# Kernel tuning notes

Measured on AMD Instinct MI355X. Metric: run time of the kernel, lower is better.

## Reference

```python
import jax, jax.numpy as jnp
import numpy as np

N_NODES = 100000
N_EDGES = 1600000
N_GRAPHS = 100
HEADS = 8
OUT_CH = 16
IN_FEAT = 128
EPS = 1e-5
NEG_SLOPE = 0.2


def setup_inputs() -> dict:
    key = jax.random.key(0)
    ks = jax.random.split(key, 8)
    x = jax.random.normal(ks[0], (N_NODES, IN_FEAT), dtype=jnp.float32)
    edge_index = jax.random.randint(ks[1], (2, N_EDGES), 0, N_NODES, dtype=jnp.int64)
    batch = jnp.sort(jax.random.randint(ks[2], (N_NODES,), 0, N_GRAPHS, dtype=jnp.int64))
    bn_gamma = jnp.ones((IN_FEAT,), jnp.float32)
    bn_beta = jnp.zeros((IN_FEAT,), jnp.float32)
    W = jax.random.normal(ks[3], (IN_FEAT, HEADS * OUT_CH), dtype=jnp.float32) * (1.0 / np.sqrt(IN_FEAT))
    att_src = jax.random.normal(ks[4], (HEADS, OUT_CH), dtype=jnp.float32) * 0.1
    att_dst = jax.random.normal(ks[5], (HEADS, OUT_CH), dtype=jnp.float32) * 0.1
    bias = jnp.zeros((OUT_CH,), jnp.float32)
    return {"x": x, "edge_index": edge_index, "batch": batch,
            "bn_gamma": bn_gamma, "bn_beta": bn_beta, "W": W,
            "att_src": att_src, "att_dst": att_dst, "bias": bias}


def reference(x, edge_index, batch, bn_gamma, bn_beta, W, att_src, att_dst, bias):
    N = x.shape[0]
    # BatchNorm1d (training mode: batch statistics, biased variance)
    mean = jnp.mean(x, axis=0)
    var = jnp.var(x, axis=0)
    xn = (x - mean) * jax.lax.rsqrt(var + EPS) * bn_gamma + bn_beta

    # GATConv (heads=HEADS, concat=False), with self-loops as in PyG default
    loop = jnp.arange(N, dtype=edge_index.dtype)
    src = jnp.concatenate([edge_index[0], loop])  # [Et]
    dst = jnp.concatenate([edge_index[1], loop])  # [Et]

    h = (xn @ W).reshape(N, HEADS, OUT_CH)  # [N,H,C]
    a_src = jnp.einsum('nhc,hc->nh', h, att_src)  # [N,H]
    a_dst = jnp.einsum('nhc,hc->nh', h, att_dst)  # [N,H]

    e = a_src[src] + a_dst[dst]  # [Et,H]
    e = jnp.where(e > 0, e, NEG_SLOPE * e)  # leaky_relu(0.2)
    # scatter-softmax over destination node (self-loops => every segment nonempty)
    m = jax.ops.segment_max(e, dst, num_segments=N)  # [N,H]
    e = jnp.exp(e - m[dst])
    s = jax.ops.segment_sum(e, dst, num_segments=N)  # [N,H]
    alpha = e / s[dst]  # [Et,H]

    msg = alpha[:, :, None] * h[src]  # [Et,H,C]
    out = jax.ops.segment_sum(msg, dst, num_segments=N)  # [N,H,C]
    out = out.mean(axis=1) + bias  # concat=False -> head mean, [N,C]

    out = jax.nn.elu(out)

    # global_mean_pool over graph ids
    sums = jax.ops.segment_sum(out, batch, num_segments=N_GRAPHS)  # [G,C]
    cnt = jax.ops.segment_sum(jnp.ones((N,), out.dtype), batch, num_segments=N_GRAPHS)
    return sums / jnp.maximum(cnt, 1.0)[:, None]
```

## Files before the change

### kernel.cpp

```cpp
#include <hip/hip_runtime.h>
#include <hip/hip_bf16.h>
#include <hip/hip_fp16.h>


#define N_NODES 100000
#define N_EDGE  1600000
#define N_ET    1700000
#define N_G     100
#define HEADS   8
#define OUTC    16
#define EPS     1e-5f
#define NEG     0.2f
#define NB_BUCKETS 391
#define BCAP    4864
#define BNB     128
#define ABB     640
#define EPB     2657
#define ESLOTS  3
#define GEMMB   1563

typedef unsigned int uint;
typedef unsigned short ushort;
typedef float f32x2 __attribute__((ext_vector_type(2)));
typedef float f32x4 __attribute__((ext_vector_type(4)));
typedef __bf16 bf16x8 __attribute__((ext_vector_type(8)));

__device__ __forceinline__ float bf2f_lo(uint u){ union{uint i; float f;} c; c.i = u << 16; return c.f; }
__device__ __forceinline__ float bf2f_hi(uint u){ union{uint i; float f;} c; c.i = u & 0xffff0000u; return c.f; }
__device__ __forceinline__ float bf2f(ushort u){ union{uint i; float f;} c; c.i = ((uint)u) << 16; return c.f; }
__device__ __forceinline__ float scrub(float v){ return (v == v) ? v : 0.f; }

__device__ __forceinline__ ushort f2bf(float f){
  union{float ff; uint u;} c; c.ff = f;
  uint u = c.u;
  if ((u & 0x7fffffffu) > 0x7f800000u) u = 0;
  return (ushort)((u + 0x7fffu + ((u >> 16) & 1u)) >> 16);
}
__device__ __forceinline__ ushort bfsan(ushort u){
  return ((ushort)(u & 0x7fffu) > (ushort)0x7f80u) ? (ushort)0 : u;
}

__device__ __forceinline__ float ldf(const void* p, int i, int f32){
  return f32 ? ((const float*)p)[i] : bf2f(((const ushort*)p)[i]);
}
__device__ __forceinline__ int ldid(const int* p, int flat, int is64){
  return is64 ? p[2 * flat] : p[flat];
}

__global__ __launch_bounds__(1024) void k_front(const void* __restrict__ xraw,
                                                float* __restrict__ stats,
                                                const int* __restrict__ ei,
                                                int* __restrict__ bcnt,
                                                uint* __restrict__ pairBuf){
  int t = threadIdx.x;
  if (blockIdx.x < BNB){
    __shared__ int cdet;
    __shared__ float red[4][1024];
    if (t == 0) cdet = 0;
    __syncthreads();
    if (t < 256){
      uint w = ((const uint*)xraw)[t]; uint el = (w >> 7) & 0xffu;
      if (el != 0 && (el < 110 || el > 140)) atomicAdd(&cdet, 1);
    }
    __syncthreads();
    int f32 = cdet > 64;
    int c = t & 63;
    int c0 = c * 2;
    int rg = t >> 6;
    float s0 = 0.f, s1 = 0.f, q0 = 0.f, q1 = 0.f;
    if (f32){
      const float2* x2 = (const float2*)xraw;
      for (int r = blockIdx.x * 16 + rg; r < N_NODES; r += BNB * 16){
        float2 v = x2[r * 64 + c];
        float f0 = scrub(v.x), f1 = scrub(v.y);
        s0 += f0; q0 += f0 * f0;
        s1 += f1; q1 += f1 * f1;
      }
    } else {
      const uint* x2 = (const uint*)xraw;
      for (int r = blockIdx.x * 16 + rg; r < N_NODES; r += BNB * 16){
        uint v = x2[r * 64 + c];
        float f0 = scrub(bf2f_lo(v)), f1 = scrub(bf2f_hi(v));
        s0 += f0; q0 += f0 * f0;
        s1 += f1; q1 += f1 * f1;
      }
    }
    red[0][t] = s0; red[1][t] = q0; red[2][t] = s1; red[3][t] = q1;
    __syncthreads();
    if (t < 64){
      s0 = 0.f; q0 = 0.f; s1 = 0.f; q1 = 0.f;
#pragma unroll
      for (int k = 0; k < 16; k++){
        s0 += red[0][t + 64 * k];
        q0 += red[1][t + 64 * k];
        s1 += red[2][t + 64 * k];
        q1 += red[3][t + 64 * k];
      }
      atomicAdd(&stats[c0],       s0);
      atomicAdd(&stats[c0+1],     s1);
      atomicAdd(&stats[128+c0],   q0);
      atomicAdd(&stats[128+c0+1], q1);
    }
  } else {
    __shared__ int hist[NB_BUCKETS];
    __shared__ int base[NB_BUCKETS];
    __shared__ int cdet2;
    int bid = blockIdx.x - BNB;
    if (t == 0) cdet2 = 0;
    for (int i = t; i < NB_BUCKETS; i += 1024) hist[i] = 0;
    __syncthreads();
    if (t < 128){ if (ei[2 * t + 1] != 0) atomicAdd(&cdet2, 1); }
    __syncthreads();
    int is64 = cdet2 < 32;
    int e0 = bid * EPB, e1 = min(e0 + EPB, N_ET);
    uint preg[ESLOTS];
    int  breg[ESLOTS];
#pragma unroll
    for (int j = 0; j < ESLOTS; j++){
      int e = e0 + t + j * 1024;
      uint pk = 0; int b = -1;
      if (e < e1){
        int s, d;
        if (e < N_EDGE){ s = ldid(ei, e, is64); d = ldid(ei, N_EDGE + e, is64); }
        else { s = d = e - N_EDGE; }
        uint dd = (uint)d; if (dd >= N_NODES) dd = 0;
        uint ss = (uint)s; if (ss >= N_NODES) ss = 0;
        b = (int)(dd >> 8);
        pk = (ss << 8) | (dd & 255u);
        atomicAdd(&hist[b], 1);
      }
      preg[j] = pk; breg[j] = b;
    }
    __syncthreads();
    for (int i = t; i < NB_BUCKETS; i += 1024){
      int c = hist[i];
      base[i] = c ? atomicAdd(&bcnt[i], c) : 0;
      hist[i] = 0;
    }
    __syncthreads();
#pragma unroll
    for (int j = 0; j < ESLOTS; j++){
      int b = breg[j];
      if (b >= 0){
        int pos = base[b] + atomicAdd(&hist[b], 1);
        if ((uint)pos < BCAP) pairBuf[(size_t)b * BCAP + pos] = preg[j];
      }
    }
  }
}

__global__ __launch_bounds__(128) void k_prep(const float* __restrict__ stats,
                                              const void* __restrict__ gamma,
                                              const void* __restrict__ beta,
                                              const void* __restrict__ W,
                                              const uint* __restrict__ x32,
                                              const int* __restrict__ b32,
                                              ushort* __restrict__ Wpb,
                                              float* __restrict__ bp,
                                              int* __restrict__ flags){
  __shared__ int cnt[2];
  __shared__ float scl8[8], shf8[8];
  int t = threadIdx.x, bid = blockIdx.x;
  if (t < 2) cnt[t] = 0;
  __syncthreads();
  { uint w = x32[t];       uint el = (w >> 7) & 0xffu;
    if (el != 0 && (el < 110 || el > 140)) atomicAdd(&cnt[0], 1); }
  { uint w = x32[t + 128]; uint el = (w >> 7) & 0xffu;
    if (el != 0 && (el < 110 || el > 140)) atomicAdd(&cnt[0], 1); }
  if (bid == 0){ if (b32[98001 + 2 * t] != 0) atomicAdd(&cnt[1], 1); }
  __syncthreads();
  int f32 = cnt[0] > 64;
  if (bid == 0 && t == 0){
    flags[0] = f32;
    flags[1] = 0;
    flags[2] = cnt[1] < 32;
    flags[3] = 0;
  }
  if (t < 8){
    int c = bid * 8 + t;
    float mean = scrub(stats[c] * (1.0f / N_NODES));
    float var  = stats[128 + c] * (1.0f / N_NODES) - mean * mean;
    if (!(var > 0.f)) var = 0.f;
    float sc = scrub(ldf(gamma, c, f32)) * rsqrtf(var + EPS);
    sc = scrub(sc);
    scl8[t] = sc;
    shf8[t] = scrub(scrub(ldf(beta, c, f32)) - mean * sc);
  }
  __syncthreads();
  float bacc = 0.f;
#pragma unroll
  for (int j = 0; j < 8; j++){
    int c = bid * 8 + j;
    float w = scrub(ldf(W, c * 128 + t, f32));
    Wpb[t * 128 + (c & 7) + (((c >> 3) ^ (t & 15)) << 3)] = f2bf(scl8[j] * w);
    bacc += shf8[j] * w;
  }
  atomicAdd(&bp[t], scrub(bacc));
}

__global__ __launch_bounds__(256) void k_gemmC(const void* __restrict__ xraw,
                                               const ushort* __restrict__ Wpb,
                                               const float* __restrict__ bp,
                                               const void* __restrict__ att_src,
                                               const void* __restrict__ att_dst,
                                               const int* __restrict__ flags,
                                               unsigned char* __restrict__ h8,
                                               __half* __restrict__ a_src16,
                                               __half* __restrict__ a_dst16,
                                               const uint* __restrict__ pairBuf,
                                               const int* __restrict__ bcnt,
                                               int* __restrict__ offsets,
                                               int* __restrict__ csr){
  __shared__ __align__(16) char smem[33792];
  __shared__ float sSL[128], sDL[128], bpL[128];
  int t = threadIdx.x;
  if (blockIdx.x < NB_BUCKETS){
    int* sscan = (int*)smem;
    int* degL  = (int*)(smem + 2048);
    int* offL  = (int*)(smem + 3072);
    int* curL  = (int*)(smem + 4096);
    int b = blockIdx.x;
    sscan[t]       = (t < NB_BUCKETS) ? min(bcnt[t], BCAP) : 0;
    sscan[t + 256] = (t + 256 < NB_BUCKETS) ? min(bcnt[t + 256], BCAP) : 0;
    degL[t] = 0;
    __syncthreads();
    for (int off = 1; off < 512; off <<= 1){
      int a0 = (t >= off) ? sscan[t - off] : 0;
      int a1 = (t + 256 >= off) ? sscan[t + 256 - off] : 0;
      __syncthreads();
      sscan[t] += a0; sscan[t + 256] += a1;
      __syncthreads();
    }
    int gbase = (b == 0) ? 0 : sscan[b - 1];
    if (b == NB_BUCKETS - 1 && t == 0) offsets[N_NODES] = sscan[NB_BUCKETS - 1];
    int cnt = min(bcnt[b], BCAP);
    const uint* run = pairBuf + (size_t)b * BCAP;
    for (int i = t; i < cnt; i += 256)
      atomicAdd(&degL[run[i] & 255u], 1);
    __syncthreads();
    int v = degL[t];
    offL[t] = v;
    __syncthreads();
    for (int off = 1; off < 256; off <<= 1){
      int add = (t >= off) ? offL[t - off] : 0;
      __syncthreads();
      offL[t] += add;
      __syncthreads();
    }
    int excl = offL[t] - v;
    int node = (b << 8) + t;
    if (node < N_NODES) offsets[node] = gbase + excl;
    offL[t] = excl;
    curL[t] = 0;
    __syncthreads();
    for (int i = t; i < cnt; i += 256){
      uint e = run[i];
      int dl = e & 255u;
      int pos = atomicAdd(&curL[dl], 1);
      csr[gbase + offL[dl] + pos] = (int)(e >> 8);
    }
  } else {
    int f32 = flags[0];
    int wv = t >> 6, l = t & 63;
    int row0 = (blockIdx.x - NB_BUCKETS) * 64;
    if (t < 128){
      sSL[t] = scrub(ldf(att_src, t, f32));
      sDL[t] = scrub(ldf(att_dst, t, f32));
      bpL[t] = bp[t];
    }
    {
      const uint4* wsrc = (const uint4*)Wpb;
      uint4* wdst = (uint4*)smem;
#pragma unroll
      for (int i = 0; i < 8; i++)
        wdst[i * 256 + t] = wsrc[i * 256 + t];
    }
    __syncthreads();
    ushort* BsT = (ushort*)smem;

    f32x4 acc[8];
#pragma unroll
    for (int ct = 0; ct < 8; ct++) acc[ct] = (f32x4){0.f, 0.f, 0.f, 0.f};
    int arow = row0 + wv * 16 + (l & 15);
    int cr = min(arow, N_NODES - 1);
    int kg = (l >> 4) * 8;
    union AB { uint4 q; bf16x8 v; ushort u[8]; };
#pragma unroll
    for (int kc = 0; kc < 4; kc++){
      AB a;
      if (f32){
        const float* xr = (const float*)xraw + (size_t)cr * 128 + kc * 32 + kg;
        float4 p0 = *(const float4*)xr;
        float4 p1 = *(const float4*)(xr + 4);
        a.u[0] = f2bf(p0.x); a.u[1] = f2bf(p0.y); a.u[2] = f2bf(p0.z); a.u[3] = f2bf(p0.w);
        a.u[4] = f2bf(p1.x); a.u[5] = f2bf(p1.y); a.u[6] = f2bf(p1.z); a.u[7] = f2bf(p1.w);
      } else {
        const ushort* xr = (const ushort*)xraw + (size_t)cr * 128 + kc * 32 + kg;
        a.q = *(const uint4*)xr;
#pragma unroll
        for (int j = 0; j < 8; j++) a.u[j] = bfsan(a.u[j]);
      }
#pragma unroll
      for (int ct = 0; ct < 8; ct++){
        int c = ct * 16 + (l & 15);
        int kb = kc * 4 + (l >> 4);
        AB bfr;
        bfr.q = *(const uint4*)(BsT + c * 128 + ((kb ^ (c & 15)) << 3));
        acc[ct] = __builtin_amdgcn_mfma_f32_16x16x32_bf16(a.v, bfr.v, acc[ct], 0, 0, 0);
      }
    }
    __syncthreads();
    float* Cs = (float*)smem;
#pragma unroll
    for (int ct = 0; ct < 8; ct++){
#pragma unroll
      for (int ri = 0; ri < 4; ri++)
        Cs[(wv * 16 + (l >> 4) * 4 + ri) * 132 + ct * 16 + (l & 15)] = acc[ct][ri];
    }
    __syncthreads();
    int row = t >> 2, cg = (t & 3) * 32;
    int r = row0 + row;
    if (r < N_NODES){
      float o[32];
#pragma unroll
      for (int i = 0; i < 8; i++){
        float4 v = *(const float4*)(Cs + row * 132 + cg + i * 4);
        o[i*4+0] = v.x; o[i*4+1] = v.y; o[i*4+2] = v.z; o[i*4+3] = v.w;
      }
#pragma unroll
      for (int j = 0; j < 32; j++){
        float v = scrub(o[j] + bpL[cg + j]);
        o[j] = fminf(fmaxf(v, -448.f), 448.f);
      }
      uint w[8];
#pragma unroll
      for (int i = 0; i < 8; i++){
        uint ww = __builtin_amdgcn_cvt_pk_fp8_f32(o[i*4+0], o[i*4+1], 0, false);
        w[i] = __builtin_amdgcn_cvt_pk_fp8_f32(o[i*4+2], o[i*4+3], (int)ww, true);
      }
      unsigned char* po = h8 + (size_t)r * 128 + cg;
      *(uint4*)po        = make_uint4(w[0], w[1], w[2], w[3]);
      *(uint4*)(po + 16) = make_uint4(w[4], w[5], w[6], w[7]);
      float s0 = 0.f, s1 = 0.f, d0 = 0.f, d1 = 0.f;
#pragma unroll
      for (int j = 0; j < 16; j++){
        s0 += o[j]      * sSL[cg + j];      d0 += o[j]      * sDL[cg + j];
        s1 += o[16 + j] * sSL[cg + 16 + j]; d1 += o[16 + j] * sDL[cg + 16 + j];
      }
      int hA = (t & 3) * 2;
      *(__half2*)(a_src16 + (size_t)r * 8 + hA) = __floats2half2_rn(scrub(s0), scrub(s1));
      *(__half2*)(a_dst16 + (size_t)r * 8 + hA) = __floats2half2_rn(scrub(d0), scrub(d1));
    }
  }
}

__global__ __launch_bounds__(256) void k_msg(const int* __restrict__ offsets, const int* __restrict__ csr,
                                             const __half* __restrict__ a_src16, const __half* __restrict__ a_dst16,
                                             const uint* __restrict__ h32, const void* __restrict__ bias,
                                             const int* __restrict__ flags,
                                             float* __restrict__ out_n){
  int f32 = flags[0];
  int t = threadIdx.x;
  int wv = t >> 6, lane = t & 63;
  int half = lane >> 5, li = lane & 31;
  int myh = li >> 2;
  int n = blockIdx.x * 4 + wv;
  int start = offsets[n], end = offsets[n + 1];
  float ad = __half2float(a_dst16[(size_t)n * 8 + myh]);
  const ushort* as16 = (const ushort*)a_src16;
  float acc0 = 0.f, acc1 = 0.f, acc2 = 0.f, acc3 = 0.f, den = 0.f;

#define PAIR(AA, HH)                                                  \
  { float e = __half2float(*(__half*)&(AA)) + ad;                     \
    e = fmaxf(e, NEG * e);                                            \
    float p = __expf(fminf(e, 30.f));                                 \
    f32x2 lo = __builtin_amdgcn_cvt_pk_f32_fp8((int)(HH), false);     \
    f32x2 hi = __builtin_amdgcn_cvt_pk_f32_fp8((int)(HH), true);      \
    den += p; acc0 += p * lo[0]; acc1 += p * lo[1];                   \
    acc2 += p * hi[0]; acc3 += p * hi[1]; }

  for (int base = start; base < end; base += 64){
    int cnt = min(64, end - base);
    int sreg = csr[min(base + lane, N_ET - 1)];
    int npair = cnt >> 1;
    int jj = 0;
    for (; jj + 4 <= npair; jj += 4){
      int i0 = 2 * jj + half;
      int s0 = __shfl(sreg, i0);
      int s1 = __shfl(sreg, i0 + 2);
      int s2 = __shfl(sreg, i0 + 4);
      int s3 = __shfl(sreg, i0 + 6);
      uint h0 = h32[(uint)s0 * 32u + li];
      uint h1 = h32[(uint)s1 * 32u + li];
      uint h2 = h32[(uint)s2 * 32u + li];
      uint h3 = h32[(uint)s3 * 32u + li];
      ushort a0 = as16[(uint)s0 * 8u + myh];
      ushort a1 = as16[(uint)s1 * 8u + myh];
      ushort a2 = as16[(uint)s2 * 8u + myh];
      ushort a3 = as16[(uint)s3 * 8u + myh];
      __builtin_amdgcn_sched_barrier(0);
      PAIR(a0, h0) PAIR(a1, h1) PAIR(a2, h2) PAIR(a3, h3)
    }
    for (; jj < npair; jj++){
      int s0 = __shfl(sreg, 2 * jj + half);
      uint h0 = h32[(uint)s0 * 32u + li];
      ushort a0 = as16[(uint)s0 * 8u + myh];
      PAIR(a0, h0)
    }
    if (cnt & 1){
      int sl = __shfl(sreg, cnt - 1);
      uint hh = h32[(uint)sl * 32u + li];
      ushort aa = as16[(uint)sl * 8u + myh];
      float e = __half2float(*(__half*)&aa) + ad;
      e = fmaxf(e, NEG * e);
      float p = __expf(fminf(e, 30.f));
      p = half ? 0.f : p;
      f32x2 lo = __builtin_amdgcn_cvt_pk_f32_fp8((int)hh, false);
      f32x2 hi = __builtin_amdgcn_cvt_pk_f32_fp8((int)hh, true);
      den += p; acc0 += p * lo[0]; acc1 += p * lo[1];
      acc2 += p * hi[0]; acc3 += p * hi[1];
    }
  }
#undef PAIR

  den  += __shfl_xor(den, 32);
  acc0 += __shfl_xor(acc0, 32);
  acc1 += __shfl_xor(acc1, 32);
  acc2 += __shfl_xor(acc2, 32);
  acc3 += __shfl_xor(acc3, 32);
  float inv = (den > 0.f) ? (1.0f / den) : 0.f;
  float v0 = acc0 * inv, v1 = acc1 * inv, v2 = acc2 * inv, v3 = acc3 * inv;
  v0 += __shfl_xor(v0, 4);  v1 += __shfl_xor(v1, 4);  v2 += __shfl_xor(v2, 4);  v3 += __shfl_xor(v3, 4);
  v0 += __shfl_xor(v0, 8);  v1 += __shfl_xor(v1, 8);  v2 += __shfl_xor(v2, 8);  v3 += __shfl_xor(v3, 8);
  v0 += __shfl_xor(v0, 16); v1 += __shfl_xor(v1, 16); v2 += __shfl_xor(v2, 16); v3 += __shfl_xor(v3, 16);
  if (lane < 4){
    int c0 = lane * 4;
    float o0 = v0 * 0.125f + scrub(ldf(bias, c0 + 0, f32));
    float o1 = v1 * 0.125f + scrub(ldf(bias, c0 + 1, f32));
    float o2 = v2 * 0.125f + scrub(ldf(bias, c0 + 2, f32));
    float o3 = v3 * 0.125f + scrub(ldf(bias, c0 + 3, f32));
    o0 = o0 > 0.f ? o0 : (__expf(o0) - 1.0f);
    o1 = o1 > 0.f ? o1 : (__expf(o1) - 1.0f);
    o2 = o2 > 0.f ? o2 : (__expf(o2) - 1.0f);
    o3 = o3 > 0.f ? o3 : (__expf(o3) - 1.0f);
    float4* po = (float4*)(out_n + (size_t)n * 16 + c0);
    *po = make_float4(scrub(o0), scrub(o1), scrub(o2), scrub(o3));
  }
}

__global__ __launch_bounds__(256) void k_pool(const float* __restrict__ out_n,
                                              const int* __restrict__ batch,
                                              const int* __restrict__ flags,
                                              float* __restrict__ out){
  int b64 = flags[2];
  int g = blockIdx.x;
  int t = threadIdx.x;
  int c = t & 15, rg = t >> 4;
  int lo = 0, hi = N_NODES;
  while (lo < hi){ int m = (lo + hi) >> 1; if (ldid(batch, m, b64) < g) lo = m + 1; else hi = m; }
  int lo2 = lo, hi2 = N_NODES;
  while (lo2 < hi2){ int m = (lo2 + hi2) >> 1; if (ldid(batch, m, b64) < g + 1) lo2 = m + 1; else hi2 = m; }
  float acc = 0.f;
  for (int r = lo + rg; r < lo2; r += 16)
    acc += out_n[(size_t)r * 16 + c];
  __shared__ float red[16][17];
  red[rg][c] = acc;
  __syncthreads();
  if (t < 16){
    float v = 0.f;
#pragma unroll
    for (int i = 0; i < 16; i++) v += red[i][t];
    float cntf = (float)(lo2 - lo);
    out[g * 16 + t] = scrub(v / fmaxf(cntf, 1.0f));
  }
}

extern "C" void kernel_launch(void* const* d_in, const int* in_sizes, int n_in,
                              void* d_out, int out_size, void* d_ws, size_t ws_size,
                              hipStream_t stream){
  (void)in_sizes; (void)n_in; (void)out_size; (void)ws_size;
  const void* x     = d_in[0];
  const int*  ei    = (const int*)d_in[1];
  const int*  batch = (const int*)d_in[2];
  const void* gamma = d_in[3];
  const void* beta  = d_in[4];
  const void* W     = d_in[5];
  const void* att_s = d_in[6];
  const void* att_d = d_in[7];
  const void* bias  = d_in[8];

  char* ws = (char*)d_ws;
  size_t off = 0;
  auto alloc = [&](size_t b){ size_t r = off; off += (b + 255) & ~(size_t)255; return r; };
  int*    flags   = (int*)(ws + alloc(4 * 4));
  float*  stats   = (float*)(ws + alloc(256 * 4));
  float*  bp      = (float*)(ws + alloc(128 * 4));
  int*    bcnt    = (int*)(ws + alloc(NB_BUCKETS * 4));
  size_t  zero_end = off;
  ushort* Wpb     = (ushort*)(ws + alloc(16384 * 2));
  int*    offsets = (int*)(ws + alloc((size_t)(N_NODES + 1) * 4));
  __half* a_src16 = (__half*)(ws + alloc((size_t)N_NODES * 8 * 2));
  __half* a_dst16 = (__half*)(ws + alloc((size_t)N_NODES * 8 * 2));
  size_t  pb_bytes = (size_t)NB_BUCKETS * BCAP * 4;
  size_t  on_bytes = (size_t)N_NODES * 16 * 4;
  char*   pb_region = ws + alloc(pb_bytes > on_bytes ? pb_bytes : on_bytes);
  uint*   pairBuf = (uint*)pb_region;
  float*  out_n   = (float*)pb_region;
  unsigned char* h8 = (unsigned char*)(ws + alloc((size_t)N_NODES * 128));
  int*    csr     = (int*)(ws + alloc((size_t)N_ET * 4));

  hipMemsetAsync(ws, 0, zero_end, stream);

  k_front<<<BNB + ABB, 1024, 0, stream>>>(x, stats, ei, bcnt, pairBuf);
  k_prep<<<16, 128, 0, stream>>>(stats, gamma, beta, W, (const uint*)x, batch, Wpb, bp, flags);
  k_gemmC<<<NB_BUCKETS + GEMMB, 256, 0, stream>>>(x, Wpb, bp, att_s, att_d, flags,
                                                  h8, a_src16, a_dst16,
                                                  pairBuf, bcnt, offsets, csr);
  k_msg<<<N_NODES / 4, 256, 0, stream>>>(offsets, csr, a_src16, a_dst16, (const uint*)h8, bias, flags, out_n);
  k_pool<<<N_G, 256, 0, stream>>>(out_n, batch, flags, (float*)d_out);
}
```

Before: 257.2 us.

## Split edge bucketing from BN stats and co-schedule it with half the GEMM

The edge-bucketing pass moves out of the BN statistics kernel into a new kernel that also runs the first half of the GEMM row tiles. The CSR build shares a launch with the remaining GEMM tiles. The bucketing blocks drop to 256 threads, each handling 12 edges with paired vectorized index loads. The aim is to overlap the memory-bound edge scatter with compute-bound GEMM work and to balance block mix across launches, at the cost of one extra launch and a split GEMM.

```diff
diff --git a/kernel.cpp b/kernel.cpp
--- a/kernel.cpp
+++ b/kernel.cpp
@@ -16,8 +16,9 @@
 #define BNB     128
 #define ABB     640
 #define EPB     2657
-#define ESLOTS  3
 #define GEMMB   1563
+#define GB1     760
+#define GB2     803
 
 typedef unsigned int uint;
 typedef unsigned short ushort;
@@ -47,105 +48,55 @@
   return is64 ? p[2 * flat] : p[flat];
 }
 
-__global__ __launch_bounds__(1024) void k_front(const void* __restrict__ xraw,
-                                                float* __restrict__ stats,
-                                                const int* __restrict__ ei,
-                                                int* __restrict__ bcnt,
-                                                uint* __restrict__ pairBuf){
+__global__ __launch_bounds__(1024) void k_bn(const void* __restrict__ xraw,
+                                             float* __restrict__ stats){
   int t = threadIdx.x;
-  if (blockIdx.x < BNB){
-    __shared__ int cdet;
-    __shared__ float red[4][1024];
-    if (t == 0) cdet = 0;
-    __syncthreads();
-    if (t < 256){
-      uint w = ((const uint*)xraw)[t]; uint el = (w >> 7) & 0xffu;
-      if (el != 0 && (el < 110 || el > 140)) atomicAdd(&cdet, 1);
-    }
-    __syncthreads();
-    int f32 = cdet > 64;
-    int c = t & 63;
-    int c0 = c * 2;
-    int rg = t >> 6;
-    float s0 = 0.f, s1 = 0.f, q0 = 0.f, q1 = 0.f;
-    if (f32){
-      const float2* x2 = (const float2*)xraw;
-      for (int r = blockIdx.x * 16 + rg; r < N_NODES; r += BNB * 16){
-        float2 v = x2[r * 64 + c];
-        float f0 = scrub(v.x), f1 = scrub(v.y);
-        s0 += f0; q0 += f0 * f0;
-        s1 += f1; q1 += f1 * f1;
-      }
-    } else {
-      const uint* x2 = (const uint*)xraw;
-      for (int r = blockIdx.x * 16 + rg; r < N_NODES; r += BNB * 16){
-        uint v = x2[r * 64 + c];
-        float f0 = scrub(bf2f_lo(v)), f1 = scrub(bf2f_hi(v));
-        s0 += f0; q0 += f0 * f0;
-        s1 += f1; q1 += f1 * f1;
-      }
-    }
-    red[0][t] = s0; red[1][t] = q0; red[2][t] = s1; red[3][t] = q1;
-    __syncthreads();
-    if (t < 64){
-      s0 = 0.f; q0 = 0.f; s1 = 0.f; q1 = 0.f;
-#pragma unroll
-      for (int k = 0; k < 16; k++){
-        s0 += red[0][t + 64 * k];
-        q0 += red[1][t + 64 * k];
-        s1 += red[2][t + 64 * k];
-        q1 += red[3][t + 64 * k];
-      }
-      atomicAdd(&stats[c0],       s0);
-      atomicAdd(&stats[c0+1],     s1);
-      atomicAdd(&stats[128+c0],   q0);
-      atomicAdd(&stats[128+c0+1], q1);
+  __shared__ int cdet;
+  __shared__ float red[4][1024];
+  if (t == 0) cdet = 0;
+  __syncthreads();
+  if (t < 256){
+    uint w = ((const uint*)xraw)[t]; uint el = (w >> 7) & 0xffu;
+    if (el != 0 && (el < 110 || el > 140)) atomicAdd(&cdet, 1);
+  }
+  __syncthreads();
+  int f32 = cdet > 64;
+  int c = t & 63;
+  int c0 = c * 2;
+  int rg = t >> 6;
+  float s0 = 0.f, s1 = 0.f, q0 = 0.f, q1 = 0.f;
+  if (f32){
+    const float2* x2 = (const float2*)xraw;
+    for (int r = blockIdx.x * 16 + rg; r < N_NODES; r += BNB * 16){
+      float2 v = x2[r * 64 + c];
+      float f0 = scrub(v.x), f1 = scrub(v.y);
+      s0 += f0; q0 += f0 * f0;
+      s1 += f1; q1 += f1 * f1;
     }
   } else {
-    __shared__ int hist[NB_BUCKETS];
-    __shared__ int base[NB_BUCKETS];
-    __shared__ int cdet2;
-    int bid = blockIdx.x - BNB;
-    if (t == 0) cdet2 = 0;
-    for (int i = t; i < NB_BUCKETS; i += 1024) hist[i] = 0;
-    __syncthreads();
-    if (t < 128){ if (ei[2 * t + 1] != 0) atomicAdd(&cdet2, 1); }
-    __syncthreads();
-    int is64 = cdet2 < 32;
-    int e0 = bid * EPB, e1 = min(e0 + EPB, N_ET);
-    uint preg[ESLOTS];
-    int  breg[ESLOTS];
-#pragma unroll
-    for (int j = 0; j < ESLOTS; j++){
-      int e = e0 + t + j * 1024;
-      uint pk = 0; int b = -1;
-      if (e < e1){
-        int s, d;
-        if (e < N_EDGE){ s = ldid(ei, e, is64); d = ldid(ei, N_EDGE + e, is64); }
-        else { s = d = e - N_EDGE; }
-        uint dd = (uint)d; if (dd >= N_NODES) dd = 0;
-        uint ss = (uint)s; if (ss >= N_NODES) ss = 0;
-        b = (int)(dd >> 8);
-        pk = (ss << 8) | (dd & 255u);
-        atomicAdd(&hist[b], 1);
-      }
-      preg[j] = pk; breg[j] = b;
-    }
-    __syncthreads();
-    for (int i = t; i < NB_BUCKETS; i += 1024){
-      int c = hist[i];
-      base[i] = c ? atomicAdd(&bcnt[i], c) : 0;
-      hist[i] = 0;
-    }
-    __syncthreads();
-#pragma unroll
-    for (int j = 0; j < ESLOTS; j++){
-      int b = breg[j];
-      if (b >= 0){
-        int pos = base[b] + atomicAdd(&hist[b], 1);
-        if ((uint)pos < BCAP) pairBuf[(size_t)b * BCAP + pos] = preg[j];
-      }
-    }
+    const uint* x2 = (const uint*)xraw;
+    for (int r = blockIdx.x * 16 + rg; r < N_NODES; r += BNB * 16){
+      uint v = x2[r * 64 + c];
+      float f0 = scrub(bf2f_lo(v)), f1 = scrub(bf2f_hi(v));
+      s0 += f0; q0 += f0 * f0;
+      s1 += f1; q1 += f1 * f1;
+    }
+  }
+  red[0][t] = s0; red[1][t] = q0; red[2][t] = s1; red[3][t] = q1;
+  __syncthreads();
+  if (t < 64){
+    s0 = 0.f; q0 = 0.f; s1 = 0.f; q1 = 0.f;
+#pragma unroll
+    for (int k = 0; k < 16; k++){
+      s0 += red[0][t + 64 * k];
+      q0 += red[1][t + 64 * k];
+      s1 += red[2][t + 64 * k];
+      q1 += red[3][t + 64 * k];
+    }
+    atomicAdd(&stats[c0],       s0);
+    atomicAdd(&stats[c0+1],     s1);
+    atomicAdd(&stats[128+c0],   q0);
+    atomicAdd(&stats[128+c0+1], q1);
   }
 }
 
@@ -198,19 +149,216 @@
   atomicAdd(&bp[t], scrub(bacc));
 }
 
-__global__ __launch_bounds__(256) void k_gemmC(const void* __restrict__ xraw,
-                                               const ushort* __restrict__ Wpb,
-                                               const float* __restrict__ bp,
-                                               const void* __restrict__ att_src,
-                                               const void* __restrict__ att_dst,
-                                               const int* __restrict__ flags,
-                                               unsigned char* __restrict__ h8,
-                                               __half* __restrict__ a_src16,
-                                               __half* __restrict__ a_dst16,
-                                               const uint* __restrict__ pairBuf,
-                                               const int* __restrict__ bcnt,
-                                               int* __restrict__ offsets,
-                                               int* __restrict__ csr){
+__device__ __forceinline__ void gemm_body(int row0, char* smem,
+                                          float* sSL, float* sDL, float* bpL,
+                                          const void* __restrict__ xraw,
+                                          const ushort* __restrict__ Wpb,
+                                          const float* __restrict__ bp,
+                                          const void* __restrict__ att_src,
+                                          const void* __restrict__ att_dst,
+                                          int f32, int t,
+                                          unsigned char* __restrict__ h8,
+                                          __half* __restrict__ a_src16,
+                                          __half* __restrict__ a_dst16){
+  int wv = t >> 6, l = t & 63;
+  if (t < 128){
+    sSL[t] = scrub(ldf(att_src, t, f32));
+    sDL[t] = scrub(ldf(att_dst, t, f32));
+    bpL[t] = bp[t];
+  }
+  {
+    const uint4* wsrc = (const uint4*)Wpb;
+    uint4* wdst = (uint4*)smem;
+#pragma unroll
+    for (int i = 0; i < 8; i++)
+      wdst[i * 256 + t] = wsrc[i * 256 + t];
+  }
+  __syncthreads();
+  ushort* BsT = (ushort*)smem;
+
+  f32x4 acc[8];
+#pragma unroll
+  for (int ct = 0; ct < 8; ct++) acc[ct] = (f32x4){0.f, 0.f, 0.f, 0.f};
+  int arow = row0 + wv * 16 + (l & 15);
+  int cr = min(arow, N_NODES - 1);
+  int kg = (l >> 4) * 8;
+  union AB { uint4 q; bf16x8 v; ushort u[8]; };
+#pragma unroll
+  for (int kc = 0; kc < 4; kc++){
+    AB a;
+    if (f32){
+      const float* xr = (const float*)xraw + (size_t)cr * 128 + kc * 32 + kg;
+      float4 p0 = *(const float4*)xr;
+      float4 p1 = *(const float4*)(xr + 4);
+      a.u[0] = f2bf(p0.x); a.u[1] = f2bf(p0.y); a.u[2] = f2bf(p0.z); a.u[3] = f2bf(p0.w);
+      a.u[4] = f2bf(p1.x); a.u[5] = f2bf(p1.y); a.u[6] = f2bf(p1.z); a.u[7] = f2bf(p1.w);
+    } else {
+      const ushort* xr = (const ushort*)xraw + (size_t)cr * 128 + kc * 32 + kg;
+      a.q = *(const uint4*)xr;
+#pragma unroll
+      for (int j = 0; j < 8; j++) a.u[j] = bfsan(a.u[j]);
+    }
+#pragma unroll
+    for (int ct = 0; ct < 8; ct++){
+      int c = ct * 16 + (l & 15);
+      int kb = kc * 4 + (l >> 4);
+      AB bfr;
+      bfr.q = *(const uint4*)(BsT + c * 128 + ((kb ^ (c & 15)) << 3));
+      acc[ct] = __builtin_amdgcn_mfma_f32_16x16x32_bf16(a.v, bfr.v, acc[ct], 0, 0, 0);
+    }
+  }
+  __syncthreads();
+  float* Cs = (float*)smem;
+#pragma unroll
+  for (int ct = 0; ct < 8; ct++){
+#pragma unroll
+    for (int ri = 0; ri < 4; ri++)
+      Cs[(wv * 16 + (l >> 4) * 4 + ri) * 132 + ct * 16 + (l & 15)] = acc[ct][ri];
+  }
+  __syncthreads();
+  int row = t >> 2, cg = (t & 3) * 32;
+  int r = row0 + row;
+  if (r < N_NODES){
+    float o[32];
+#pragma unroll
+    for (int i = 0; i < 8; i++){
+      float4 v = *(const float4*)(Cs + row * 132 + cg + i * 4);
+      o[i*4+0] = v.x; o[i*4+1] = v.y; o[i*4+2] = v.z; o[i*4+3] = v.w;
+    }
+#pragma unroll
+    for (int j = 0; j < 32; j++){
+      float v = scrub(o[j] + bpL[cg + j]);
+      o[j] = fminf(fmaxf(v, -448.f), 448.f);
+    }
+    uint w[8];
+#pragma unroll
+    for (int i = 0; i < 8; i++){
+      uint ww = __builtin_amdgcn_cvt_pk_fp8_f32(o[i*4+0], o[i*4+1], 0, false);
+      w[i] = __builtin_amdgcn_cvt_pk_fp8_f32(o[i*4+2], o[i*4+3], (int)ww, true);
+    }
+    unsigned char* po = h8 + (size_t)r * 128 + cg;
+    *(uint4*)po        = make_uint4(w[0], w[1], w[2], w[3]);
+    *(uint4*)(po + 16) = make_uint4(w[4], w[5], w[6], w[7]);
+    float s0 = 0.f, s1 = 0.f, d0 = 0.f, d1 = 0.f;
+#pragma unroll
+    for (int j = 0; j < 16; j++){
+      s0 += o[j]      * sSL[cg + j];      d0 += o[j]      * sDL[cg + j];
+      s1 += o[16 + j] * sSL[cg + 16 + j]; d1 += o[16 + j] * sDL[cg + 16 + j];
+    }
+    int hA = (t & 3) * 2;
+    *(__half2*)(a_src16 + (size_t)r * 8 + hA) = __floats2half2_rn(scrub(s0), scrub(s1));
+    *(__half2*)(a_dst16 + (size_t)r * 8 + hA) = __floats2half2_rn(scrub(d0), scrub(d1));
+  }
+}
+
+__global__ __launch_bounds__(256) void k_AB1(const void* __restrict__ xraw,
+                                             const ushort* __restrict__ Wpb,
+                                             const float* __restrict__ bp,
+                                             const void* __restrict__ att_src,
+                                             const void* __restrict__ att_dst,
+                                             const int* __restrict__ flags,
+                                             unsigned char* __restrict__ h8,
+                                             __half* __restrict__ a_src16,
+                                             __half* __restrict__ a_dst16,
+                                             const int* __restrict__ ei,
+                                             int* __restrict__ bcnt,
+                                             uint* __restrict__ pairBuf){
+  __shared__ __align__(16) char smem[33792];
+  __shared__ float sSL[128], sDL[128], bpL[128];
+  __shared__ int cdet2;
+  int t = threadIdx.x;
+  if (blockIdx.x < ABB){
+    int* hist = (int*)smem;
+    int* base = (int*)(smem + 1664);
+    int bid = blockIdx.x;
+    if (t == 0) cdet2 = 0;
+    for (int i = t; i < NB_BUCKETS; i += 256) hist[i] = 0;
+    __syncthreads();
+    if (t < 128){ if (ei[2 * t + 1] != 0) atomicAdd(&cdet2, 1); }
+    __syncthreads();
+    int is64 = cdet2 < 32;
+    int e0 = bid * EPB, e1 = min(e0 + EPB, N_ET);
+    uint pk[12]; int bk[12];
+#pragma unroll
+    for (int j = 0; j < 6; j++){
+      int e = e0 + 2 * (t + j * 256);
+      int s0v = 0, d0v = 0, s1v = 0, d1v = 0;
+      bool v0 = e < e1, v1 = (e + 1) < e1;
+      if (v0 && (e + 1 < N_EDGE)){
+        if (is64){
+          uint4 sv = *(const uint4*)(ei + 4 * (size_t)e);
+          uint4 dv = *(const uint4*)(ei + 4 * ((size_t)N_EDGE + e));
+          s0v = (int)sv.x; s1v = (int)sv.z;
+          d0v = (int)dv.x; d1v = (int)dv.z;
+        } else {
+          uint2 sv = *(const uint2*)((const uint*)ei + e);
+          uint2 dv = *(const uint2*)((const uint*)ei + N_EDGE + e);
+          s0v = (int)sv.x; s1v = (int)sv.y;
+          d0v = (int)dv.x; d1v = (int)dv.y;
+        }
+      } else {
+        if (v0){
+          if (e < N_EDGE){ s0v = ldid(ei, e, is64); d0v = ldid(ei, N_EDGE + e, is64); }
+          else { s0v = d0v = e - N_EDGE; }
+        }
+        if (v1){
+          int e2 = e + 1;
+          if (e2 < N_EDGE){ s1v = ldid(ei, e2, is64); d1v = ldid(ei, N_EDGE + e2, is64); }
+          else { s1v = d1v = e2 - N_EDGE; }
+        }
+      }
+      uint p0 = 0; int b0 = -1;
+      if (v0){
+        uint dd = (uint)d0v; if (dd >= N_NODES) dd = 0;
+        uint ss = (uint)s0v; if (ss >= N_NODES) ss = 0;
+        b0 = (int)(dd >> 8); p0 = (ss << 8) | (dd & 255u);
+        atomicAdd(&hist[b0], 1);
+      }
+      pk[2*j] = p0; bk[2*j] = b0;
+      uint p1 = 0; int b1 = -1;
+      if (v1){
+        uint dd = (uint)d1v; if (dd >= N_NODES) dd = 0;
+        uint ss = (uint)s1v; if (ss >= N_NODES) ss = 0;
+        b1 = (int)(dd >> 8); p1 = (ss << 8) | (dd & 255u);
+        atomicAdd(&hist[b1], 1);
+      }
+      pk[2*j+1] = p1; bk[2*j+1] = b1;
+    }
+    __syncthreads();
+    for (int i = t; i < NB_BUCKETS; i += 256){
+      int c = hist[i];
+      base[i] = c ? atomicAdd(&bcnt[i], c) : 0;
+      hist[i] = 0;
+    }
+    __syncthreads();
+#pragma unroll
+    for (int j = 0; j < 12; j++){
+      int b = bk[j];
+      if (b >= 0){
+        int pos = base[b] + atomicAdd(&hist[b], 1);
+        if ((uint)pos < BCAP) pairBuf[(size_t)b * BCAP + pos] = pk[j];
+      }
+    }
+  } else {
+    gemm_body((blockIdx.x - ABB) * 64, smem, sSL, sDL, bpL,
+              xraw, Wpb, bp, att_src, att_dst, flags[0], t,
+              h8, a_src16, a_dst16);
+  }
+}
+
+__global__ __launch_bounds__(256) void k_C2(const void* __restrict__ xraw,
+                                            const ushort* __restrict__ Wpb,
+                                            const float* __restrict__ bp,
+                                            const void* __restrict__ att_src,
+                                            const void* __restrict__ att_dst,
+                                            const int* __restrict__ flags,
+                                            unsigned char* __restrict__ h8,
+                                            __half* __restrict__ a_src16,
+                                            __half* __restrict__ a_dst16,
+                                            const uint* __restrict__ pairBuf,
+                                            const int* __restrict__ bcnt,
+                                            int* __restrict__ offsets,
+                                            int* __restrict__ csr){
   __shared__ __align__(16) char smem[33792];
   __shared__ float sSL[128], sDL[128], bpL[128];
   int t = threadIdx.x;
@@ -260,97 +408,9 @@
       csr[gbase + offL[dl] + pos] = (int)(e >> 8);
     }
   } else {
-    int f32 = flags[0];
-    int wv = t >> 6, l = t & 63;
-    int row0 = (blockIdx.x - NB_BUCKETS) * 64;
-    if (t < 128){
-      sSL[t] = scrub(ldf(att_src, t, f32));
-      sDL[t] = scrub(ldf(att_dst, t, f32));
-      bpL[t] = bp[t];
-    }
-    {
-      const uint4* wsrc = (const uint4*)Wpb;
-      uint4* wdst = (uint4*)smem;
-#pragma unroll
-      for (int i = 0; i < 8; i++)
-        wdst[i * 256 + t] = wsrc[i * 256 + t];
-    }
-    __syncthreads();
-    ushort* BsT = (ushort*)smem;
-
-    f32x4 acc[8];
-#pragma unroll
-    for (int ct = 0; ct < 8; ct++) acc[ct] = (f32x4){0.f, 0.f, 0.f, 0.f};
-    int arow = row0 + wv * 16 + (l & 15);
-    int cr = min(arow, N_NODES - 1);
-    int kg = (l >> 4) * 8;
-    union AB { uint4 q; bf16x8 v; ushort u[8]; };
-#pragma unroll
-    for (int kc = 0; kc < 4; kc++){
-      AB a;
-      if (f32){
-        const float* xr = (const float*)xraw + (size_t)cr * 128 + kc * 32 + kg;
-        float4 p0 = *(const float4*)xr;
-        float4 p1 = *(const float4*)(xr + 4);
-        a.u[0] = f2bf(p0.x); a.u[1] = f2bf(p0.y); a.u[2] = f2bf(p0.z); a.u[3] = f2bf(p0.w);
-        a.u[4] = f2bf(p1.x); a.u[5] = f2bf(p1.y); a.u[6] = f2bf(p1.z); a.u[7] = f2bf(p1.w);
-      } else {
-        const ushort* xr = (const ushort*)xraw + (size_t)cr * 128 + kc * 32 + kg;
-        a.q = *(const uint4*)xr;
-#pragma unroll
-        for (int j = 0; j < 8; j++) a.u[j] = bfsan(a.u[j]);
-      }
-#pragma unroll
-      for (int ct = 0; ct < 8; ct++){
-        int c = ct * 16 + (l & 15);
-        int kb = kc * 4 + (l >> 4);
-        AB bfr;
-        bfr.q = *(const uint4*)(BsT + c * 128 + ((kb ^ (c & 15)) << 3));
-        acc[ct] = __builtin_amdgcn_mfma_f32_16x16x32_bf16(a.v, bfr.v, acc[ct], 0, 0, 0);
-      }
-    }
-    __syncthreads();
-    float* Cs = (float*)smem;
-#pragma unroll
-    for (int ct = 0; ct < 8; ct++){
-#pragma unroll
-      for (int ri = 0; ri < 4; ri++)
-        Cs[(wv * 16 + (l >> 4) * 4 + ri) * 132 + ct * 16 + (l & 15)] = acc[ct][ri];
-    }
-    __syncthreads();
-    int row = t >> 2, cg = (t & 3) * 32;
-    int r = row0 + row;
-    if (r < N_NODES){
-      float o[32];
-#pragma unroll
-      for (int i = 0; i < 8; i++){
-        float4 v = *(const float4*)(Cs + row * 132 + cg + i * 4);
-        o[i*4+0] = v.x; o[i*4+1] = v.y; o[i*4+2] = v.z; o[i*4+3] = v.w;
-      }
-#pragma unroll
-      for (int j = 0; j < 32; j++){
-        float v = scrub(o[j] + bpL[cg + j]);
-        o[j] = fminf(fmaxf(v, -448.f), 448.f);
-      }
-      uint w[8];
-#pragma unroll
-      for (int i = 0; i < 8; i++){
-        uint ww = __builtin_amdgcn_cvt_pk_fp8_f32(o[i*4+0], o[i*4+1], 0, false);
-        w[i] = __builtin_amdgcn_cvt_pk_fp8_f32(o[i*4+2], o[i*4+3], (int)ww, true);
-      }
-      unsigned char* po = h8 + (size_t)r * 128 + cg;
-      *(uint4*)po        = make_uint4(w[0], w[1], w[2], w[3]);
-      *(uint4*)(po + 16) = make_uint4(w[4], w[5], w[6], w[7]);
-      float s0 = 0.f, s1 = 0.f, d0 = 0.f, d1 = 0.f;
-#pragma unroll
-      for (int j = 0; j < 16; j++){
-        s0 += o[j]      * sSL[cg + j];      d0 += o[j]      * sDL[cg + j];
-        s1 += o[16 + j] * sSL[cg + 16 + j]; d1 += o[16 + j] * sDL[cg + 16 + j];
-      }
-      int hA = (t & 3) * 2;
-      *(__half2*)(a_src16 + (size_t)r * 8 + hA) = __floats2half2_rn(scrub(s0), scrub(s1));
-      *(__half2*)(a_dst16 + (size_t)r * 8 + hA) = __floats2half2_rn(scrub(d0), scrub(d1));
-    }
+    gemm_body(GB1 * 64 + (blockIdx.x - NB_BUCKETS) * 64, smem, sSL, sDL, bpL,
+              xraw, Wpb, bp, att_src, att_dst, flags[0], t,
+              h8, a_src16, a_dst16);
   }
 }
 
@@ -511,11 +571,13 @@
 
   hipMemsetAsync(ws, 0, zero_end, stream);
 
-  k_front<<<BNB + ABB, 1024, 0, stream>>>(x, stats, ei, bcnt, pairBuf);
+  k_bn<<<BNB, 1024, 0, stream>>>(x, stats);
   k_prep<<<16, 128, 0, stream>>>(stats, gamma, beta, W, (const uint*)x, batch, Wpb, bp, flags);
-  k_gemmC<<<NB_BUCKETS + GEMMB, 256, 0, stream>>>(x, Wpb, bp, att_s, att_d, flags,
-                                                  h8, a_src16, a_dst16,
-                                                  pairBuf, bcnt, offsets, csr);
+  k_AB1<<<ABB + GB1, 256, 0, stream>>>(x, Wpb, bp, att_s, att_d, flags,
+                                       h8, a_src16, a_dst16, ei, bcnt, pairBuf);
+  k_C2<<<NB_BUCKETS + GB2, 256, 0, stream>>>(x, Wpb, bp, att_s, att_d, flags,
+                                             h8, a_src16, a_dst16,
+                                             pairBuf, bcnt, offsets, csr);
   k_msg<<<N_NODES / 4, 256, 0, stream>>>(offsets, csr, a_src16, a_dst16, (const uint*)h8, bias, flags, out_n);
   k_pool<<<N_G, 256, 0, stream>>>(out_n, batch, flags, (float*)d_out);
 }
```

Result: slower. 271.3 us (+5.5%).
